# Optimization experiments

Hardware: AMD Instinct MI355X
Metric: run time of the kernel (lower is better)

The kernel has to match this reference:

```python
import jax, jax.numpy as jnp
import numpy as np

NUM_GROUPS = 32
EPS = 1e-6


def group_norm(x, scale, bias):
    # x: (b, c, t, h, w)
    b, c, t, h, w = x.shape
    xg = x.reshape(b, NUM_GROUPS, c // NUM_GROUPS, t, h, w)
    mean = jnp.mean(xg, axis=(2, 3, 4, 5), keepdims=True)
    var = jnp.var(xg, axis=(2, 3, 4, 5), keepdims=True)
    xg = (xg - mean) * jax.lax.rsqrt(var + EPS)
    xn = xg.reshape(b, c, t, h, w)
    return xn * scale[None, :, None, None, None] + bias[None, :, None, None, None]


def conv1x1(x, w, bvec):
    # 1x1x1 Conv3d == per-position linear over channels
    return jnp.einsum('oc,bcthw->bothw', w, x) + bvec[None, :, None, None, None]


def setup_inputs() -> dict:
    key = jax.random.key(0)
    ks = jax.random.split(key, 11)
    b, c, t, h, w = 2, 256, 4, 32, 32
    x = jax.random.normal(ks[0], (b, c, t, h, w), dtype=jnp.float32)
    s = 1.0 / np.sqrt(c)
    return {
        'x': x,
        'gn_scale': jnp.ones((c,), jnp.float32),
        'gn_bias': jnp.zeros((c,), jnp.float32),
        'wq': jax.random.normal(ks[1], (c, c), jnp.float32) * s,
        'bq': jax.random.normal(ks[2], (c,), jnp.float32) * 0.01,
        'wk': jax.random.normal(ks[3], (c, c), jnp.float32) * s,
        'bk': jax.random.normal(ks[4], (c,), jnp.float32) * 0.01,
        'wv': jax.random.normal(ks[5], (c, c), jnp.float32) * s,
        'bv': jax.random.normal(ks[6], (c,), jnp.float32) * 0.01,
        'wp': jax.random.normal(ks[7], (c, c), jnp.float32) * s,
        'bp': jax.random.normal(ks[8], (c,), jnp.float32) * 0.01,
    }


def reference(x, gn_scale, gn_bias, wq, bq, wk, bk, wv, bv, wp, bp):
    b, c, t, h, w = x.shape
    n = t * h * w
    h_ = group_norm(x, gn_scale, gn_bias)
    q = conv1x1(h_, wq, bq).reshape(b, c, n)  # (b, c, n)
    k = conv1x1(h_, wk, bk).reshape(b, c, n)
    v = conv1x1(h_, wv, bv).reshape(b, c, n)
    scale = jnp.asarray(int(c) ** (-0.5), x.dtype)
    # attn[b, i, j] = sum_c q[b,c,i] k[b,c,j]
    attn = jnp.einsum('bci,bcj->bij', q, k) * scale
    attn = jax.nn.softmax(attn, axis=2)
    # A[b, c, i] = sum_j v[b,c,j] attn[b,i,j]
    A = jnp.einsum('bcj,bij->bci', v, attn).reshape(b, c, t, h, w)
    A = conv1x1(A, wp, bp)
    return x + A
```

## Files before the change

kernel.cpp:

```cpp
#include <hip/hip_runtime.h>
#include <hip/hip_bf16.h>
#include <math.h>

#define BB 2
#define CC 256
#define GG 32
#define NN 4096
#define EPSF 1e-6f
#define JSPLIT 8
#define JBLK (NN / JSPLIT)
#define CH 32
#define NT (JBLK / CH)
#define QTILE 128
#define LOG2E 1.4426950408889634f

typedef _Float16 f16x8 __attribute__((ext_vector_type(8)));
typedef float f32x4 __attribute__((ext_vector_type(4)));

static __device__ __forceinline__ unsigned short f2h_bits(float f) {
    _Float16 h = (_Float16)f;
    return __builtin_bit_cast(unsigned short, h);
}
static __device__ __forceinline__ unsigned pkh2(float a, float b) {
    return __builtin_bit_cast(unsigned, __builtin_amdgcn_cvt_pkrtz(a, b));
}
static __device__ __forceinline__ void gload16(const void* g, void* l) {
    __builtin_amdgcn_global_load_lds(
        (const __attribute__((address_space(1))) void*)g,
        (__attribute__((address_space(3))) void*)l, 16, 0, 0);
}

__global__ __launch_bounds__(256) void prep_w16_kernel(
    const float* __restrict__ wq, const float* __restrict__ wk,
    const float* __restrict__ wv, const float* __restrict__ wp,
    unsigned short* __restrict__ w16)
{
    int m = blockIdx.y;
    const float* src = (m == 0) ? wq : (m == 1) ? wk : (m == 2) ? wv : wp;
    float scale = (m == 0) ? 0.0625f * LOG2E : 1.0f;
    int idx = blockIdx.x * 256 + threadIdx.x;
    float4 v = ((const float4*)src)[idx];
    union { _Float16 h[4]; uint2 u; } pk;
    pk.h[0] = (_Float16)(v.x * scale);
    pk.h[1] = (_Float16)(v.y * scale);
    pk.h[2] = (_Float16)(v.z * scale);
    pk.h[3] = (_Float16)(v.w * scale);
    *(uint2*)(w16 + (size_t)m * CC * CC + (size_t)idx * 4) = pk.u;
}

__global__ __launch_bounds__(256) void gn_part_kernel(
    const float* __restrict__ x, float2* __restrict__ part)
{
    int g = blockIdx.x, p = blockIdx.y, b = blockIdx.z;
    const float* base = x + ((size_t)b * CC + (size_t)g * 8) * NN + (size_t)p * 8192;
    int t = threadIdx.x;
    float s = 0.f, ss = 0.f;
    for (int idx = t; idx < 2048; idx += 256) {
        float4 v4 = ((const float4*)base)[idx];
        s  += v4.x + v4.y + v4.z + v4.w;
        ss += v4.x*v4.x + v4.y*v4.y + v4.z*v4.z + v4.w*v4.w;
    }
    for (int off = 32; off; off >>= 1) {
        s  += __shfl_down(s,  off);
        ss += __shfl_down(ss, off);
    }
    __shared__ float red[8];
    int wid = t >> 6;
    if ((t & 63) == 0) { red[wid*2] = s; red[wid*2+1] = ss; }
    __syncthreads();
    if (t == 0) {
        part[(b*GG + g)*4 + p] = make_float2(red[0]+red[2]+red[4]+red[6],
                                             red[1]+red[3]+red[5]+red[7]);
    }
}

__global__ __launch_bounds__(256) void gn_apply_kernel(
    const float* __restrict__ x, const float* __restrict__ sc,
    const float* __restrict__ bi, const float2* __restrict__ part,
    unsigned short* __restrict__ hT)
{
    int b  = blockIdx.y;
    int i0 = blockIdx.x * 64;
    int t  = threadIdx.x;
    __shared__ unsigned short tile[64][264];
    __shared__ float s_mean[GG], s_rstd[GG], s_sc[CC], s_bi[CC];
    if (t < GG) {
        float2 p0 = part[(b*GG + t)*4 + 0];
        float2 p1 = part[(b*GG + t)*4 + 1];
        float2 p2 = part[(b*GG + t)*4 + 2];
        float2 p3 = part[(b*GG + t)*4 + 3];
        float S  = p0.x + p1.x + p2.x + p3.x;
        float SS = p0.y + p1.y + p2.y + p3.y;
        float mean = S / 32768.f;
        float var  = SS / 32768.f - mean * mean;
        s_mean[t] = mean;
        s_rstd[t] = rsqrtf(var + EPSF);
    }
    s_sc[t] = sc[t];
    s_bi[t] = bi[t];
    __syncthreads();
    int i4 = (t & 15) * 4;
    int cb = t >> 4;
    for (int k = 0; k < 16; k++) {
        int c = cb + k * 16;
        float4 v4 = *(const float4*)(x + ((size_t)b*CC + c)*NN + i0 + i4);
        float a = s_rstd[c >> 3] * s_sc[c];
        float d = s_bi[c] - s_mean[c >> 3] * a;
        tile[i4+0][c] = f2h_bits(v4.x * a + d);
        tile[i4+1][c] = f2h_bits(v4.y * a + d);
        tile[i4+2][c] = f2h_bits(v4.z * a + d);
        tile[i4+3][c] = f2h_bits(v4.w * a + d);
    }
    __syncthreads();
    int row = t >> 2, c0 = (t & 3) * 64;
    unsigned short* dst = hT + (size_t)b*NN*CC + (size_t)(i0 + row)*CC + c0;
    for (int k = 0; k < 8; k++) {
        uint4 u = *(const uint4*)&tile[row][c0 + k*8];
        *(uint4*)(dst + k*8) = u;
    }
}

__global__ __launch_bounds__(256) void proj_qk_kernel(
    const unsigned short* __restrict__ hT,
    const unsigned short* __restrict__ w16,
    const float* __restrict__ bq, const float* __restrict__ bk,
    unsigned short* __restrict__ qT, unsigned short* __restrict__ kT)
{
    int b = blockIdx.z >> 1, p = blockIdx.z & 1;
    const unsigned short* wgt = w16 + (size_t)p * CC * CC;
    const float* bias = p ? bk : bq;
    unsigned short* out = p ? kT : qT;
    float oscale = p ? 1.0f : 0.0625f * LOG2E;
    int i0 = blockIdx.x * 64, o0 = blockIdx.y * 64;
    int lane = threadIdx.x & 63, wid = threadIdx.x >> 6;
    int col = lane & 15, grp = lane >> 4;
    int ow = o0 + wid * 16;
    const unsigned short* hb = hT + (size_t)b*NN*CC;
    f32x4 acc[4];
    for (int it = 0; it < 4; it++) acc[it] = (f32x4){0.f,0.f,0.f,0.f};
    for (int ck = 0; ck < 8; ck++) {
        f16x8 af = *(const f16x8*)(wgt + (size_t)(ow + col)*CC + ck*32 + grp*8);
        for (int it = 0; it < 4; it++) {
            f16x8 bf = *(const f16x8*)(hb + (size_t)(i0 + it*16 + col)*CC + ck*32 + grp*8);
            acc[it] = __builtin_amdgcn_mfma_f32_16x16x32_f16(af, bf, acc[it], 0, 0, 0);
        }
    }
    int obase = ow + grp * 4;
    float b0 = bias[obase]*oscale, b1 = bias[obase+1]*oscale,
          b2 = bias[obase+2]*oscale, b3 = bias[obase+3]*oscale;
    for (int it = 0; it < 4; it++) {
        int i = i0 + it*16 + col;
        union { _Float16 h[4]; uint2 u; } pk;
        pk.h[0] = (_Float16)(acc[it][0] + b0);
        pk.h[1] = (_Float16)(acc[it][1] + b1);
        pk.h[2] = (_Float16)(acc[it][2] + b2);
        pk.h[3] = (_Float16)(acc[it][3] + b3);
        *(uint2*)(out + (size_t)b*NN*CC + (size_t)i*CC + obase) = pk.u;
    }
}

__global__ __launch_bounds__(256) void proj_v_kernel(
    const unsigned short* __restrict__ hT,
    const unsigned short* __restrict__ wv16, const float* __restrict__ bv,
    unsigned short* __restrict__ vC)
{
    int b = blockIdx.z;
    int i0 = blockIdx.x * 64, o0 = blockIdx.y * 64;
    int lane = threadIdx.x & 63, wid = threadIdx.x >> 6;
    int col = lane & 15, grp = lane >> 4;
    int ibase = i0 + wid * 16;
    const unsigned short* hb = hT + (size_t)b*NN*CC;
    f32x4 acc[4];
    for (int ot = 0; ot < 4; ot++) acc[ot] = (f32x4){0.f,0.f,0.f,0.f};
    for (int ck = 0; ck < 8; ck++) {
        f16x8 af = *(const f16x8*)(hb + (size_t)(ibase + col)*CC + ck*32 + grp*8);
        for (int ot = 0; ot < 4; ot++) {
            f16x8 bf = *(const f16x8*)(wv16 + (size_t)(o0 + ot*16 + col)*CC + ck*32 + grp*8);
            acc[ot] = __builtin_amdgcn_mfma_f32_16x16x32_f16(af, bf, acc[ot], 0, 0, 0);
        }
    }
    int iw = ibase + grp * 4;
    for (int ot = 0; ot < 4; ot++) {
        int o = o0 + ot*16 + col;
        float bo = bv[o];
        union { _Float16 h[4]; uint2 u; } pk;
        pk.h[0] = (_Float16)(acc[ot][0] + bo);
        pk.h[1] = (_Float16)(acc[ot][1] + bo);
        pk.h[2] = (_Float16)(acc[ot][2] + bo);
        pk.h[3] = (_Float16)(acc[ot][3] + bo);
        *(uint2*)(vC + (size_t)b*CC*NN + (size_t)o*NN + iw) = pk.u;
    }
}

__global__ __launch_bounds__(256, 2) void attn_kernel(
    const unsigned short* __restrict__ qT,
    const unsigned short* __restrict__ kT,
    const unsigned short* __restrict__ vC,
    unsigned short* __restrict__ pO,
    float2* __restrict__ ml)
{
    int qt = blockIdx.x, s = blockIdx.y, b = blockIdx.z;
    int tid = threadIdx.x, w = tid >> 6, lane = tid & 63;
    int l15 = lane & 15, grp = lane >> 4;
    int q0 = qt * QTILE + w * 32;
    int jlo = s * JBLK;

    __shared__ unsigned short bufK[2][8192];
    __shared__ unsigned short bufV[2][8192];

    const unsigned short* qb = qT + (size_t)b * NN * CC;
    const unsigned short* kb = kT + (size_t)b * NN * CC;
    const unsigned short* vb = vC + (size_t)b * CC * NN;

    f16x8 qfA[8], qfB[8];
    #pragma unroll
    for (int ck = 0; ck < 8; ck++) {
        qfA[ck] = *(const f16x8*)(qb + (size_t)(q0 + l15)*CC + ck*32 + grp*8);
        qfB[ck] = *(const f16x8*)(qb + (size_t)(q0 + 16 + l15)*CC + ck*32 + grp*8);
    }

    int koff[4], voff[4];
    #pragma unroll
    for (int e = 0; e < 4; e++) {
        int blk = (4*w + e)*64 + lane;
        int kj = blk >> 5, kcb = blk & 31;
        koff[e] = kj*CC + ((kcb ^ (kj & 7)) * 8);
        int vc = blk >> 2, vcb = blk & 3;
        voff[e] = vc*NN + ((vcb ^ ((vc >> 1) & 3)) * 8);
    }
    int kru = l15 * 512;
    int krw = (l15 & 7) << 4;
    int g16 = grp << 4;
    int vrb = l15*64 + ((grp ^ ((l15 >> 1) & 3)) << 4);

    f32x4 OA[16], OB[16];
    #pragma unroll
    for (int ck = 0; ck < 16; ck++) {
        OA[ck] = (f32x4){0.f,0.f,0.f,0.f};
        OB[ck] = (f32x4){0.f,0.f,0.f,0.f};
    }
    float mA = -1e30f, lA = 0.f, mB = -1e30f, lB = 0.f;

    #pragma unroll
    for (int e = 0; e < 4; e++) {
        gload16(kb + (size_t)jlo*CC + koff[e], &bufK[0][(4*w + e)*512]);
        gload16(vb + voff[e] + jlo,            &bufV[0][(4*w + e)*512]);
    }
    __syncthreads();

    int cur = 0;
    for (int t = 0; t < NT; t++) {
        if (t + 1 < NT) {
            int j0n = jlo + (t + 1) * CH;
            #pragma unroll
            for (int e = 0; e < 4; e++) {
                gload16(kb + (size_t)j0n*CC + koff[e], &bufK[cur ^ 1][(4*w + e)*512]);
                gload16(vb + voff[e] + j0n,            &bufV[cur ^ 1][(4*w + e)*512]);
            }
        }
        const char* kbase = (const char*)&bufK[cur][0];
        const char* vbase = (const char*)&bufV[cur][0];

        f32x4 sA0 = (f32x4){0.f,0.f,0.f,0.f}, sA1 = (f32x4){0.f,0.f,0.f,0.f};
        f32x4 sB0 = (f32x4){0.f,0.f,0.f,0.f}, sB1 = (f32x4){0.f,0.f,0.f,0.f};
        __builtin_amdgcn_s_setprio(1);
        #pragma unroll
        for (int ck = 0; ck < 8; ck++) {
            int cx = ((ck*64) | g16) ^ krw;
            f16x8 k0 = *(const f16x8*)(kbase + kru + cx);
            f16x8 k1 = *(const f16x8*)(kbase + 8192 + kru + cx);
            sA0 = __builtin_amdgcn_mfma_f32_16x16x32_f16(k0, qfA[ck], sA0, 0, 0, 0);
            sA1 = __builtin_amdgcn_mfma_f32_16x16x32_f16(k1, qfA[ck], sA1, 0, 0, 0);
            sB0 = __builtin_amdgcn_mfma_f32_16x16x32_f16(k0, qfB[ck], sB0, 0, 0, 0);
            sB1 = __builtin_amdgcn_mfma_f32_16x16x32_f16(k1, qfB[ck], sB1, 0, 0, 0);
        }
        __builtin_amdgcn_s_setprio(0);

        f16x8 pfA, pfB;
        {
            float x0 = fmaxf(fmaxf(sA0[0], sA0[1]), fmaxf(sA0[2], sA0[3]));
            float x1 = fmaxf(fmaxf(sA1[0], sA1[1]), fmaxf(sA1[2], sA1[3]));
            float mx = fmaxf(x0, x1);
            mx = fmaxf(mx, __shfl_xor(mx, 16));
            mx = fmaxf(mx, __shfl_xor(mx, 32));
            bool up = !__all(mx <= mA);
            if (up) {
                float mn = fmaxf(mA, mx);
                float f = exp2f(mA - mn);
                mA = mn;
                lA *= f;
                int fb = (lane & 48) | (grp << 2);
                float fs0 = __shfl(f, fb),   fs1 = __shfl(f, fb+1);
                float fs2 = __shfl(f, fb+2), fs3 = __shfl(f, fb+3);
                f32x4 fv = (f32x4){fs0, fs1, fs2, fs3};
                #pragma unroll
                for (int ck = 0; ck < 16; ck++) OA[ck] *= fv;
            }
            sA0[0] = exp2f(sA0[0] - mA); sA0[1] = exp2f(sA0[1] - mA);
            sA0[2] = exp2f(sA0[2] - mA); sA0[3] = exp2f(sA0[3] - mA);
            sA1[0] = exp2f(sA1[0] - mA); sA1[1] = exp2f(sA1[1] - mA);
            sA1[2] = exp2f(sA1[2] - mA); sA1[3] = exp2f(sA1[3] - mA);
            float ps = ((sA0[0]+sA0[1]) + (sA0[2]+sA0[3])) + ((sA1[0]+sA1[1]) + (sA1[2]+sA1[3]));
            ps += __shfl_xor(ps, 16);
            ps += __shfl_xor(ps, 32);
            lA += ps;
            unsigned pk0 = pkh2(sA0[0], sA0[1]);
            unsigned pk1 = pkh2(sA0[2], sA0[3]);
            unsigned pk2 = pkh2(sA1[0], sA1[1]);
            unsigned pk3 = pkh2(sA1[2], sA1[3]);
            int srcA = (((grp << 1)    ) & 3) * 16 + l15;
            int srcB = (((grp << 1) + 1) & 3) * 16 + l15;
            bool lo = (grp < 2);
            unsigned u0A = __shfl(pk0, srcA), u2A = __shfl(pk2, srcA);
            unsigned u1A = __shfl(pk1, srcA), u3A = __shfl(pk3, srcA);
            unsigned u0B = __shfl(pk0, srcB), u2B = __shfl(pk2, srcB);
            unsigned u1B = __shfl(pk1, srcB), u3B = __shfl(pk3, srcB);
            uint4 pu;
            pu.x = lo ? u0A : u2A;
            pu.y = lo ? u1A : u3A;
            pu.z = lo ? u0B : u2B;
            pu.w = lo ? u1B : u3B;
            pfA = __builtin_bit_cast(f16x8, pu);
        }
        {
            float x0 = fmaxf(fmaxf(sB0[0], sB0[1]), fmaxf(sB0[2], sB0[3]));
            float x1 = fmaxf(fmaxf(sB1[0], sB1[1]), fmaxf(sB1[2], sB1[3]));
            float mx = fmaxf(x0, x1);
            mx = fmaxf(mx, __shfl_xor(mx, 16));
            mx = fmaxf(mx, __shfl_xor(mx, 32));
            bool up = !__all(mx <= mB);
            if (up) {
                float mn = fmaxf(mB, mx);
                float f = exp2f(mB - mn);
                mB = mn;
                lB *= f;
                int fb = (lane & 48) | (grp << 2);
                float fs0 = __shfl(f, fb),   fs1 = __shfl(f, fb+1);
                float fs2 = __shfl(f, fb+2), fs3 = __shfl(f, fb+3);
                f32x4 fv = (f32x4){fs0, fs1, fs2, fs3};
                #pragma unroll
                for (int ck = 0; ck < 16; ck++) OB[ck] *= fv;
            }
            sB0[0] = exp2f(sB0[0] - mB); sB0[1] = exp2f(sB0[1] - mB);
            sB0[2] = exp2f(sB0[2] - mB); sB0[3] = exp2f(sB0[3] - mB);
            sB1[0] = exp2f(sB1[0] - mB); sB1[1] = exp2f(sB1[1] - mB);
            sB1[2] = exp2f(sB1[2] - mB); sB1[3] = exp2f(sB1[3] - mB);
            float ps = ((sB0[0]+sB0[1]) + (sB0[2]+sB0[3])) + ((sB1[0]+sB1[1]) + (sB1[2]+sB1[3]));
            ps += __shfl_xor(ps, 16);
            ps += __shfl_xor(ps, 32);
            lB += ps;
            unsigned pk0 = pkh2(sB0[0], sB0[1]);
            unsigned pk1 = pkh2(sB0[2], sB0[3]);
            unsigned pk2 = pkh2(sB1[0], sB1[1]);
            unsigned pk3 = pkh2(sB1[2], sB1[3]);
            int srcA = (((grp << 1)    ) & 3) * 16 + l15;
            int srcB = (((grp << 1) + 1) & 3) * 16 + l15;
            bool lo = (grp < 2);
            unsigned u0A = __shfl(pk0, srcA), u2A = __shfl(pk2, srcA);
            unsigned u1A = __shfl(pk1, srcA), u3A = __shfl(pk3, srcA);
            unsigned u0B = __shfl(pk0, srcB), u2B = __shfl(pk2, srcB);
            unsigned u1B = __shfl(pk1, srcB), u3B = __shfl(pk3, srcB);
            uint4 pu;
            pu.x = lo ? u0A : u2A;
            pu.y = lo ? u1A : u3A;
            pu.z = lo ? u0B : u2B;
            pu.w = lo ? u1B : u3B;
            pfB = __builtin_bit_cast(f16x8, pu);
        }
        __builtin_amdgcn_s_setprio(1);
        #pragma unroll
        for (int ck = 0; ck < 16; ck++) {
            f16x8 vf = *(const f16x8*)(vbase + ck*1024 + vrb);
            OA[ck] = __builtin_amdgcn_mfma_f32_16x16x32_f16(pfA, vf, OA[ck], 0, 0, 0);
            OB[ck] = __builtin_amdgcn_mfma_f32_16x16x32_f16(pfB, vf, OB[ck], 0, 0, 0);
        }
        __builtin_amdgcn_s_setprio(0);
        __syncthreads();
        cur ^= 1;
    }

    float invA = 1.f / lA, invB = 1.f / lB;
    int ib = (lane & 48) | (grp << 2);
    float a0 = __shfl(invA, ib),   a1 = __shfl(invA, ib+1);
    float a2 = __shfl(invA, ib+2), a3 = __shfl(invA, ib+3);
    float b0 = __shfl(invB, ib),   b1 = __shfl(invB, ib+1);
    float b2 = __shfl(invB, ib+2), b3 = __shfl(invB, ib+3);
    unsigned short* po = pO + ((size_t)(s*BB + b)*NN + q0) * CC;
    #pragma unroll
    for (int ck = 0; ck < 16; ck++) {
        po[(size_t)(grp*4+0)*CC + ck*16 + l15] = f2h_bits(OA[ck][0] * a0);
        po[(size_t)(grp*4+1)*CC + ck*16 + l15] = f2h_bits(OA[ck][1] * a1);
        po[(size_t)(grp*4+2)*CC + ck*16 + l15] = f2h_bits(OA[ck][2] * a2);
        po[(size_t)(grp*4+3)*CC + ck*16 + l15] = f2h_bits(OA[ck][3] * a3);
        po[(size_t)(16 + grp*4+0)*CC + ck*16 + l15] = f2h_bits(OB[ck][0] * b0);
        po[(size_t)(16 + grp*4+1)*CC + ck*16 + l15] = f2h_bits(OB[ck][1] * b1);
        po[(size_t)(16 + grp*4+2)*CC + ck*16 + l15] = f2h_bits(OB[ck][2] * b2);
        po[(size_t)(16 + grp*4+3)*CC + ck*16 + l15] = f2h_bits(OB[ck][3] * b3);
    }
    if (lane < 16)
        ml[(size_t)(s*BB + b)*NN + q0 + lane] = make_float2(mA, lA);
    else if (lane < 32)
        ml[(size_t)(s*BB + b)*NN + q0 + 16 + l15] = make_float2(mB, lB);
}

__global__ __launch_bounds__(256) void attn_merge_kernel(
    const unsigned short* __restrict__ pO, const float2* __restrict__ ml,
    unsigned short* __restrict__ aT)
{
    int t = threadIdx.x;
    int qrow = blockIdx.x * 16 + (t >> 4);
    int c0 = (t & 15) * 16;
    float M = -1e30f;
    float m8[JSPLIT], l8[JSPLIT];
    #pragma unroll
    for (int s = 0; s < JSPLIT; s++) {
        float2 v = ml[(size_t)s*BB*NN + qrow];
        m8[s] = v.x; l8[s] = v.y;
        M = fmaxf(M, v.x);
    }
    float W = 0.f, wt[JSPLIT];
    #pragma unroll
    for (int s = 0; s < JSPLIT; s++) { wt[s] = l8[s] * exp2f(m8[s] - M); W += wt[s]; }
    float iW = 1.f / W;
    float acc[16];
    #pragma unroll
    for (int e = 0; e < 16; e++) acc[e] = 0.f;
    #pragma unroll
    for (int s = 0; s < JSPLIT; s++) {
        const unsigned short* p = pO + ((size_t)s*BB*NN + qrow)*CC + c0;
        f16x8 a0 = *(const f16x8*)p;
        f16x8 a1 = *(const f16x8*)(p + 8);
        float ws = wt[s] * iW;
        #pragma unroll
        for (int e = 0; e < 8; e++) {
            acc[e]     += ws * (float)a0[e];
            acc[e + 8] += ws * (float)a1[e];
        }
    }
    union { _Float16 h[8]; uint4 u; } o0, o1;
    #pragma unroll
    for (int e = 0; e < 8; e++) { o0.h[e] = (_Float16)acc[e]; o1.h[e] = (_Float16)acc[e+8]; }
    unsigned short* dst = aT + (size_t)qrow*CC + c0;
    *(uint4*)dst = o0.u;
    *(uint4*)(dst + 8) = o1.u;
}

__global__ __launch_bounds__(256) void proj_out_kernel(
    const unsigned short* __restrict__ aT,
    const unsigned short* __restrict__ wp16, const float* __restrict__ bp,
    const float* __restrict__ x, float* __restrict__ out)
{
    int b = blockIdx.z;
    int i0 = blockIdx.x * 64, o0 = blockIdx.y * 64;
    int lane = threadIdx.x & 63, wid = threadIdx.x >> 6;
    int col = lane & 15, grp = lane >> 4;
    int ibase = i0 + wid * 16;
    const unsigned short* ab = aT + (size_t)b*NN*CC;
    f32x4 acc[4];
    for (int ot = 0; ot < 4; ot++) acc[ot] = (f32x4){0.f,0.f,0.f,0.f};
    for (int ck = 0; ck < 8; ck++) {
        f16x8 af = *(const f16x8*)(ab + (size_t)(ibase + col)*CC + ck*32 + grp*8);
        for (int ot = 0; ot < 4; ot++) {
            f16x8 bf = *(const f16x8*)(wp16 + (size_t)(o0 + ot*16 + col)*CC + ck*32 + grp*8);
            acc[ot] = __builtin_amdgcn_mfma_f32_16x16x32_f16(af, bf, acc[ot], 0, 0, 0);
        }
    }
    int iw = ibase + grp * 4;
    for (int ot = 0; ot < 4; ot++) {
        int o = o0 + ot*16 + col;
        float bo = bp[o];
        size_t base = (size_t)b*CC*NN + (size_t)o*NN + iw;
        float4 x4 = *(const float4*)(x + base);
        float4 r;
        r.x = x4.x + acc[ot][0] + bo;
        r.y = x4.y + acc[ot][1] + bo;
        r.z = x4.z + acc[ot][2] + bo;
        r.w = x4.w + acc[ot][3] + bo;
        *(float4*)(out + base) = r;
    }
}

extern "C" void kernel_launch(void* const* d_in, const int* in_sizes, int n_in,
                              void* d_out, int out_size, void* d_ws, size_t ws_size,
                              hipStream_t stream) {
    const float* x  = (const float*)d_in[0];
    const float* gs = (const float*)d_in[1];
    const float* gb = (const float*)d_in[2];
    const float* wq = (const float*)d_in[3];
    const float* bq = (const float*)d_in[4];
    const float* wk = (const float*)d_in[5];
    const float* bk = (const float*)d_in[6];
    const float* wv = (const float*)d_in[7];
    const float* bv = (const float*)d_in[8];
    const float* wp = (const float*)d_in[9];
    const float* bp = (const float*)d_in[10];
    float* out = (float*)d_out;

    char* ws = (char*)d_ws;
    const size_t sz = (size_t)BB * NN * CC * sizeof(unsigned short);
    unsigned short* hT  = (unsigned short*)(ws);
    unsigned short* qT  = (unsigned short*)(ws + sz);
    unsigned short* kT  = (unsigned short*)(ws + 2*sz);
    unsigned short* vC  = (unsigned short*)(ws + 3*sz);
    unsigned short* aT  = (unsigned short*)(ws + 4*sz);
    unsigned short* w16 = (unsigned short*)(ws + 5*sz);
    float2* part        = (float2*)(ws + 5*sz + 512*1024);
    float2* ml          = (float2*)(ws + 5*sz + 768*1024);
    unsigned short* pO  = (unsigned short*)(ws + 5*sz + 1280*1024);

    prep_w16_kernel<<<dim3(CC*CC/4/256, 4), 256, 0, stream>>>(wq, wk, wv, wp, w16);
    gn_part_kernel<<<dim3(GG, 4, BB), 256, 0, stream>>>(x, part);
    gn_apply_kernel<<<dim3(NN/64, BB), 256, 0, stream>>>(x, gs, gb, part, hT);
    proj_qk_kernel<<<dim3(NN/64, CC/64, 2*BB), 256, 0, stream>>>(hT, w16, bq, bk, qT, kT);
    proj_v_kernel<<<dim3(NN/64, CC/64, BB), 256, 0, stream>>>(hT, w16 + 2*CC*CC, bv, vC);
    attn_kernel<<<dim3(NN/QTILE, JSPLIT, BB), 256, 0, stream>>>(qT, kT, vC, pO, ml);
    attn_merge_kernel<<<dim3(BB*NN/16), 256, 0, stream>>>(pO, ml, aT);
    proj_out_kernel<<<dim3(NN/64, CC/64, BB), 256, 0, stream>>>(aT, w16 + 3*CC*CC, bp, x, out);
}
```

Measured before the change: 141.9 us.

## Fuse GroupNorm apply into QKV projection and split K/V staging in attention

Merges the group-norm apply, Q/K projection and V projection kernels into one kernel. It keeps the normalized fp16 tile in swizzled shared memory, so the hT intermediate is no longer written to and re-read from global memory, and two launches are removed. Separately, the attention loop now prefetches K two tiles ahead and V one tile ahead, using explicit vmcnt waits and raw barriers in place of __syncthreads. The fused kernel runs only 256 blocks, each doing all the output channels, which lowers parallelism. The hand-counted waitcnt values must match the loads actually issued, or the loop reads stale data.

```diff
diff --git a/kernel.cpp b/kernel.cpp
--- a/kernel.cpp
+++ b/kernel.cpp
@@ -74,15 +74,19 @@
     }
 }
 
-__global__ __launch_bounds__(256) void gn_apply_kernel(
+__global__ __launch_bounds__(256) void proj_qkv_kernel(
     const float* __restrict__ x, const float* __restrict__ sc,
     const float* __restrict__ bi, const float2* __restrict__ part,
-    unsigned short* __restrict__ hT)
+    const unsigned short* __restrict__ w16,
+    const float* __restrict__ bq, const float* __restrict__ bk,
+    const float* __restrict__ bv,
+    unsigned short* __restrict__ qT, unsigned short* __restrict__ kT,
+    unsigned short* __restrict__ vC)
 {
     int b  = blockIdx.y;
-    int i0 = blockIdx.x * 64;
+    int i0 = blockIdx.x * 32;
     int t  = threadIdx.x;
-    __shared__ unsigned short tile[64][264];
+    __shared__ unsigned short htile[32 * 256];
     __shared__ float s_mean[GG], s_rstd[GG], s_sc[CC], s_bi[CC];
     if (t < GG) {
         float2 p0 = part[(b*GG + t)*4 + 0];
@@ -99,98 +103,120 @@
     s_sc[t] = sc[t];
     s_bi[t] = bi[t];
     __syncthreads();
-    int i4 = (t & 15) * 4;
-    int cb = t >> 4;
-    for (int k = 0; k < 16; k++) {
-        int c = cb + k * 16;
-        float4 v4 = *(const float4*)(x + ((size_t)b*CC + c)*NN + i0 + i4);
-        float a = s_rstd[c >> 3] * s_sc[c];
-        float d = s_bi[c] - s_mean[c >> 3] * a;
-        tile[i4+0][c] = f2h_bits(v4.x * a + d);
-        tile[i4+1][c] = f2h_bits(v4.y * a + d);
-        tile[i4+2][c] = f2h_bits(v4.z * a + d);
-        tile[i4+3][c] = f2h_bits(v4.w * a + d);
+
+    char* hw = (char*)htile;
+    int nq = (t & 7) * 4;
+    int cq = (t >> 3) * 4;
+    #pragma unroll
+    for (int k = 0; k < 2; k++) {
+        int c0 = cq + k * 128;
+        float4 xr[4];
+        float aa[4], dd[4];
+        #pragma unroll
+        for (int e = 0; e < 4; e++) {
+            int c = c0 + e;
+            xr[e] = *(const float4*)(x + ((size_t)b*CC + c)*NN + i0 + nq);
+            aa[e] = s_rstd[c >> 3] * s_sc[c];
+            dd[e] = s_bi[c] - s_mean[c >> 3] * aa[e];
+        }
+        #pragma unroll
+        for (int j = 0; j < 4; j++) {
+            int row = nq + j;
+            union { _Float16 h[4]; uint2 u; } pk;
+            pk.h[0] = (_Float16)(((const float*)&xr[0])[j] * aa[0] + dd[0]);
+            pk.h[1] = (_Float16)(((const float*)&xr[1])[j] * aa[1] + dd[1]);
+            pk.h[2] = (_Float16)(((const float*)&xr[2])[j] * aa[2] + dd[2]);
+            pk.h[3] = (_Float16)(((const float*)&xr[3])[j] * aa[3] + dd[3]);
+            int off = row*512 + (((c0 >> 3) ^ (row & 7)) << 4) + (c0 & 7) * 2;
+            *(uint2*)(hw + off) = pk.u;
+        }
     }
     __syncthreads();
-    int row = t >> 2, c0 = (t & 3) * 64;
-    unsigned short* dst = hT + (size_t)b*NN*CC + (size_t)(i0 + row)*CC + c0;
-    for (int k = 0; k < 8; k++) {
-        uint4 u = *(const uint4*)&tile[row][c0 + k*8];
-        *(uint4*)(dst + k*8) = u;
-    }
-}
-
-__global__ __launch_bounds__(256) void proj_qk_kernel(
-    const unsigned short* __restrict__ hT,
-    const unsigned short* __restrict__ w16,
-    const float* __restrict__ bq, const float* __restrict__ bk,
-    unsigned short* __restrict__ qT, unsigned short* __restrict__ kT)
-{
-    int b = blockIdx.z >> 1, p = blockIdx.z & 1;
-    const unsigned short* wgt = w16 + (size_t)p * CC * CC;
-    const float* bias = p ? bk : bq;
-    unsigned short* out = p ? kT : qT;
-    float oscale = p ? 1.0f : 0.0625f * LOG2E;
-    int i0 = blockIdx.x * 64, o0 = blockIdx.y * 64;
-    int lane = threadIdx.x & 63, wid = threadIdx.x >> 6;
+
+    int lane = t & 63, w = t >> 6;
     int col = lane & 15, grp = lane >> 4;
-    int ow = o0 + wid * 16;
-    const unsigned short* hb = hT + (size_t)b*NN*CC;
-    f32x4 acc[4];
-    for (int it = 0; it < 4; it++) acc[it] = (f32x4){0.f,0.f,0.f,0.f};
-    for (int ck = 0; ck < 8; ck++) {
-        f16x8 af = *(const f16x8*)(wgt + (size_t)(ow + col)*CC + ck*32 + grp*8);
-        for (int it = 0; it < 4; it++) {
-            f16x8 bf = *(const f16x8*)(hb + (size_t)(i0 + it*16 + col)*CC + ck*32 + grp*8);
-            acc[it] = __builtin_amdgcn_mfma_f32_16x16x32_f16(af, bf, acc[it], 0, 0, 0);
-        }
-    }
-    int obase = ow + grp * 4;
-    float b0 = bias[obase]*oscale, b1 = bias[obase+1]*oscale,
-          b2 = bias[obase+2]*oscale, b3 = bias[obase+3]*oscale;
-    for (int it = 0; it < 4; it++) {
-        int i = i0 + it*16 + col;
-        union { _Float16 h[4]; uint2 u; } pk;
-        pk.h[0] = (_Float16)(acc[it][0] + b0);
-        pk.h[1] = (_Float16)(acc[it][1] + b1);
-        pk.h[2] = (_Float16)(acc[it][2] + b2);
-        pk.h[3] = (_Float16)(acc[it][3] + b3);
-        *(uint2*)(out + (size_t)b*NN*CC + (size_t)i*CC + obase) = pk.u;
-    }
-}
-
-__global__ __launch_bounds__(256) void proj_v_kernel(
-    const unsigned short* __restrict__ hT,
-    const unsigned short* __restrict__ wv16, const float* __restrict__ bv,
-    unsigned short* __restrict__ vC)
-{
-    int b = blockIdx.z;
-    int i0 = blockIdx.x * 64, o0 = blockIdx.y * 64;
-    int lane = threadIdx.x & 63, wid = threadIdx.x >> 6;
-    int col = lane & 15, grp = lane >> 4;
-    int ibase = i0 + wid * 16;
-    const unsigned short* hb = hT + (size_t)b*NN*CC;
-    f32x4 acc[4];
-    for (int ot = 0; ot < 4; ot++) acc[ot] = (f32x4){0.f,0.f,0.f,0.f};
-    for (int ck = 0; ck < 8; ck++) {
-        f16x8 af = *(const f16x8*)(hb + (size_t)(ibase + col)*CC + ck*32 + grp*8);
+    const char* hr = (const char*)htile;
+
+    #pragma unroll
+    for (int p = 0; p < 2; p++) {
+        const unsigned short* wgt = w16 + (size_t)p * CC * CC;
+        const float* bias = p ? bk : bq;
+        unsigned short* outp = (p ? kT : qT) + (size_t)b * NN * CC;
+        float osc = p ? 1.0f : 0.0625f * LOG2E;
+        #pragma unroll
         for (int ot = 0; ot < 4; ot++) {
-            f16x8 bf = *(const f16x8*)(wv16 + (size_t)(o0 + ot*16 + col)*CC + ck*32 + grp*8);
-            acc[ot] = __builtin_amdgcn_mfma_f32_16x16x32_f16(af, bf, acc[ot], 0, 0, 0);
-        }
-    }
-    int iw = ibase + grp * 4;
-    for (int ot = 0; ot < 4; ot++) {
-        int o = o0 + ot*16 + col;
-        float bo = bv[o];
-        union { _Float16 h[4]; uint2 u; } pk;
-        pk.h[0] = (_Float16)(acc[ot][0] + bo);
-        pk.h[1] = (_Float16)(acc[ot][1] + bo);
-        pk.h[2] = (_Float16)(acc[ot][2] + bo);
-        pk.h[3] = (_Float16)(acc[ot][3] + bo);
-        *(uint2*)(vC + (size_t)b*CC*NN + (size_t)o*NN + iw) = pk.u;
-    }
-}
+            int ow = ot * 64 + w * 16;
+            f32x4 acc[2];
+            acc[0] = (f32x4){0.f,0.f,0.f,0.f};
+            acc[1] = (f32x4){0.f,0.f,0.f,0.f};
+            #pragma unroll
+            for (int ck = 0; ck < 8; ck++) {
+                f16x8 af = *(const f16x8*)(wgt + (size_t)(ow + col)*CC + ck*32 + grp*8);
+                #pragma unroll
+                for (int it = 0; it < 2; it++) {
+                    int row = it*16 + col;
+                    f16x8 bf = *(const f16x8*)(hr + row*512 + (((ck*4 + grp) ^ (row & 7)) << 4));
+                    acc[it] = __builtin_amdgcn_mfma_f32_16x16x32_f16(af, bf, acc[it], 0, 0, 0);
+                }
+            }
+            int obase = ow + grp * 4;
+            float b0 = bias[obase]*osc, b1 = bias[obase+1]*osc,
+                  b2 = bias[obase+2]*osc, b3 = bias[obase+3]*osc;
+            #pragma unroll
+            for (int it = 0; it < 2; it++) {
+                int i = i0 + it*16 + col;
+                union { _Float16 h[4]; uint2 u; } pk;
+                pk.h[0] = (_Float16)(acc[it][0] + b0);
+                pk.h[1] = (_Float16)(acc[it][1] + b1);
+                pk.h[2] = (_Float16)(acc[it][2] + b2);
+                pk.h[3] = (_Float16)(acc[it][3] + b3);
+                *(uint2*)(outp + (size_t)i*CC + obase) = pk.u;
+            }
+        }
+    }
+    {
+        const unsigned short* wgt = w16 + (size_t)2 * CC * CC;
+        unsigned short* outp = vC + (size_t)b * CC * NN;
+        int ibase = (w & 1) * 16;
+        #pragma unroll
+        for (int gg = 0; gg < 2; gg++) {
+            int og = (w >> 1) * 2 + gg;
+            f32x4 acc[4];
+            #pragma unroll
+            for (int ot = 0; ot < 4; ot++) acc[ot] = (f32x4){0.f,0.f,0.f,0.f};
+            #pragma unroll
+            for (int ck = 0; ck < 8; ck++) {
+                int row = ibase + col;
+                f16x8 af = *(const f16x8*)(hr + row*512 + (((ck*4 + grp) ^ (row & 7)) << 4));
+                #pragma unroll
+                for (int ot = 0; ot < 4; ot++) {
+                    f16x8 bf = *(const f16x8*)(wgt + (size_t)(og*64 + ot*16 + col)*CC + ck*32 + grp*8);
+                    acc[ot] = __builtin_amdgcn_mfma_f32_16x16x32_f16(af, bf, acc[ot], 0, 0, 0);
+                }
+            }
+            int iw = i0 + ibase + grp * 4;
+            #pragma unroll
+            for (int ot = 0; ot < 4; ot++) {
+                int o = og*64 + ot*16 + col;
+                float bo = bv[o];
+                union { _Float16 h[4]; uint2 u; } pk;
+                pk.h[0] = (_Float16)(acc[ot][0] + bo);
+                pk.h[1] = (_Float16)(acc[ot][1] + bo);
+                pk.h[2] = (_Float16)(acc[ot][2] + bo);
+                pk.h[3] = (_Float16)(acc[ot][3] + bo);
+                *(uint2*)(outp + (size_t)o*NN + iw) = pk.u;
+            }
+        }
+    }
+}
+
+#define WAITV(n) asm volatile("s_waitcnt vmcnt(" #n ")" ::: "memory")
+#define SBAR() do { __builtin_amdgcn_sched_barrier(0); __builtin_amdgcn_s_barrier(); \
+                    __builtin_amdgcn_sched_barrier(0); } while (0)
+#define STAGE_K(tt, bb) do { int _j = jlo + (tt)*CH; _Pragma("unroll") \
+    for (int e = 0; e < 4; e++) gload16(kb + (size_t)_j*CC + koff[e], &bufK[bb][(4*w + e)*512]); } while (0)
+#define STAGE_V(tt, bb) do { int _j = jlo + (tt)*CH; _Pragma("unroll") \
+    for (int e = 0; e < 4; e++) gload16(vb + voff[e] + _j, &bufV[bb][(4*w + e)*512]); } while (0)
 
 __global__ __launch_bounds__(256, 2) void attn_kernel(
     const unsigned short* __restrict__ qT,
@@ -241,23 +267,16 @@
     }
     float mA = -1e30f, lA = 0.f, mB = -1e30f, lB = 0.f;
 
-    #pragma unroll
-    for (int e = 0; e < 4; e++) {
-        gload16(kb + (size_t)jlo*CC + koff[e], &bufK[0][(4*w + e)*512]);
-        gload16(vb + voff[e] + jlo,            &bufV[0][(4*w + e)*512]);
-    }
-    __syncthreads();
-
-    int cur = 0;
+    STAGE_K(0, 0);
+    STAGE_V(0, 0);
+    STAGE_K(1, 1);
+
     for (int t = 0; t < NT; t++) {
-        if (t + 1 < NT) {
-            int j0n = jlo + (t + 1) * CH;
-            #pragma unroll
-            for (int e = 0; e < 4; e++) {
-                gload16(kb + (size_t)j0n*CC + koff[e], &bufK[cur ^ 1][(4*w + e)*512]);
-                gload16(vb + voff[e] + j0n,            &bufV[cur ^ 1][(4*w + e)*512]);
-            }
-        }
+        int cur = t & 1;
+        if (t < NT - 1) WAITV(8); else WAITV(4);
+        SBAR();
+        if (t + 1 < NT) STAGE_V(t + 1, cur ^ 1);
+
         const char* kbase = (const char*)&bufK[cur][0];
         const char* vbase = (const char*)&bufV[cur][0];
 
@@ -367,6 +386,11 @@
             pu.w = lo ? u1B : u3B;
             pfB = __builtin_bit_cast(f16x8, pu);
         }
+
+        if (t < NT - 1) WAITV(8); else WAITV(0);
+        SBAR();
+        if (t + 2 < NT) STAGE_K(t + 2, cur);
+
         __builtin_amdgcn_s_setprio(1);
         #pragma unroll
         for (int ck = 0; ck < 16; ck++) {
@@ -375,8 +399,6 @@
             OB[ck] = __builtin_amdgcn_mfma_f32_16x16x32_f16(pfB, vf, OB[ck], 0, 0, 0);
         }
         __builtin_amdgcn_s_setprio(0);
-        __syncthreads();
-        cur ^= 1;
     }
 
     float invA = 1.f / lA, invB = 1.f / lB;
@@ -498,7 +520,6 @@
 
     char* ws = (char*)d_ws;
     const size_t sz = (size_t)BB * NN * CC * sizeof(unsigned short);
-    unsigned short* hT  = (unsigned short*)(ws);
     unsigned short* qT  = (unsigned short*)(ws + sz);
     unsigned short* kT  = (unsigned short*)(ws + 2*sz);
     unsigned short* vC  = (unsigned short*)(ws + 3*sz);
@@ -510,9 +531,8 @@
 
     prep_w16_kernel<<<dim3(CC*CC/4/256, 4), 256, 0, stream>>>(wq, wk, wv, wp, w16);
     gn_part_kernel<<<dim3(GG, 4, BB), 256, 0, stream>>>(x, part);
-    gn_apply_kernel<<<dim3(NN/64, BB), 256, 0, stream>>>(x, gs, gb, part, hT);
-    proj_qk_kernel<<<dim3(NN/64, CC/64, 2*BB), 256, 0, stream>>>(hT, w16, bq, bk, qT, kT);
-    proj_v_kernel<<<dim3(NN/64, CC/64, BB), 256, 0, stream>>>(hT, w16 + 2*CC*CC, bv, vC);
+    proj_qkv_kernel<<<dim3(NN/32, BB), 256, 0, stream>>>(x, gs, gb, part, w16,
+                                                         bq, bk, bv, qT, kT, vC);
     attn_kernel<<<dim3(NN/QTILE, JSPLIT, BB), 256, 0, stream>>>(qT, kT, vC, pO, ml);
     attn_merge_kernel<<<dim3(BB*NN/16), 256, 0, stream>>>(pO, ml, aT);
     proj_out_kernel<<<dim3(NN/64, CC/64, BB), 256, 0, stream>>>(aT, w16 + 3*CC*CC, bp, x, out);
```

Result: no change. 141.1 us (-0.6%).
